# Performance work log

Hardware: AMD Instinct MI355X
Metric: run time of the kernel (lower is better)

## Reference

```python
import jax, jax.numpy as jnp
import numpy as np

MAX_POS = 8192
SOFT_CAP = 5.0


def rms_norm(x, scale, eps=1e-6):
    # RMSBatchNorm approximated as RMS normalization over channels with learned scale
    return x * jax.lax.rsqrt(jnp.mean(x * x, axis=-1, keepdims=True) + eps) * scale


def layer_norm(x, scale, offset, eps=1e-5):
    mean = jnp.mean(x, axis=-1, keepdims=True)
    var = jnp.mean(jnp.square(x - mean), axis=-1, keepdims=True)
    return (x - mean) * jax.lax.rsqrt(var + eps) * scale + offset


def apply_rope(x, max_position=MAX_POS):
    # x: [B, S, H, C]
    B, S, H, C = x.shape
    positions = jnp.arange(S, dtype=x.dtype).reshape(1, S)
    num_freq = C // 2
    inv_freq = (1.0 / (jnp.arange(num_freq) + jnp.geomspace(1, max_position - num_freq + 1, num_freq))).astype(x.dtype)
    theta = jnp.einsum('bs,f->bsf', positions, inv_freq)
    theta = jnp.repeat(theta, 2, axis=-1)[..., None, :]  # [1, S, 1, C]
    x_rotated = jnp.stack([-x[..., 1::2], x[..., ::2]], axis=-1).reshape(x.shape)
    return x * jnp.cos(theta) + x_rotated * jnp.sin(theta)


def setup_inputs() -> dict:
    key = jax.random.key(0)
    ks = jax.random.split(key, 16)
    B, S, D = 2, 2048, 1536
    H, CQK, CV = 8, 128, 192
    inp = {
        'x': jax.random.normal(ks[0], (B, S, D), jnp.float32),
        'attention_bias': jax.random.normal(ks[1], (B, H, S, S), jnp.float32),
        'rms_in_scale': jnp.ones((D,), jnp.float32),
        'wq': jax.random.normal(ks[2], (D, H * CQK), jnp.float32) / np.sqrt(D),
        'wk': jax.random.normal(ks[3], (D, CQK), jnp.float32) / np.sqrt(D),
        'wv': jax.random.normal(ks[4], (D, CV), jnp.float32) / np.sqrt(D),
        'q_scale': jnp.ones((CQK,), jnp.float32),
        'q_offset': jnp.zeros((CQK,), jnp.float32),
        'k_scale': jnp.ones((CQK,), jnp.float32),
        'k_offset': jnp.zeros((CQK,), jnp.float32),
        'v_scale': jnp.ones((CV,), jnp.float32),
        'v_offset': jnp.zeros((CV,), jnp.float32),
        'wo': jax.random.normal(ks[5], (H * CV, D), jnp.float32) / np.sqrt(H * CV),
        'bo': jnp.zeros((D,), jnp.float32),
        'rms_out_scale': jnp.ones((D,), jnp.float32),
    }
    return inp


def reference(x, attention_bias, rms_in_scale, wq, wk, wv, q_scale, q_offset,
              k_scale, k_offset, v_scale, v_offset, wo, bo, rms_out_scale):
    B, S, D = x.shape
    H, CQK, CV = 8, 128, 192
    h = rms_norm(x, rms_in_scale)
    q = layer_norm((h @ wq).reshape(B, S, H, CQK), q_scale, q_offset)
    k = layer_norm((h @ wk).reshape(B, S, 1, CQK), k_scale, k_offset)
    v = layer_norm((h @ wv).reshape(B, S, 1, CV), v_scale, v_offset)
    q = apply_rope(q)
    k = apply_rope(k)
    # MQA logits: single shared K head
    logits = jnp.einsum('bshc,bSc->bhsS', q, k[:, :, 0], preferred_element_type=jnp.float32)
    logits = logits / np.sqrt(128.0)
    logits = (logits + attention_bias).astype(jnp.float32)
    logits = jnp.tanh(logits / SOFT_CAP) * SOFT_CAP
    weights = jax.nn.softmax(logits, axis=-1)
    y = jnp.einsum('bhsS,bSc->bshc', weights, v[:, :, 0]).astype(q.dtype)
    y = y.reshape(B, S, H * CV) @ wo + bo
    return rms_norm(y, rms_out_scale)
```

## Files before the change

### kernel.cpp

```cpp
#include <hip/hip_runtime.h>
#include <hip/hip_bf16.h>

typedef unsigned short u16;
typedef short bf16x8 __attribute__((ext_vector_type(8)));
typedef float f32x4 __attribute__((ext_vector_type(4)));

#define NB 2
#define NS 2048
#define ND 1536
#define NH 8
#define NCQK 128
#define NCV 192
#define NBS 4096
#define NPAD 1408

__device__ __forceinline__ float bf2f(u16 u) {
  unsigned v = ((unsigned)u) << 16;
  return __builtin_bit_cast(float, v);
}
__device__ __forceinline__ u16 f2bf(float f) {
  unsigned u = __builtin_bit_cast(unsigned, f);
  u += 0x7fffu + ((u >> 16) & 1u);
  return (u16)(u >> 16);
}
__device__ __forceinline__ void glds16(const u16* g, u16* l) {
  __builtin_amdgcn_global_load_lds(
      (const __attribute__((address_space(1))) void*)g,
      (__attribute__((address_space(3))) void*)l, 16, 0, 0);
}
__device__ __forceinline__ f32x4 mfma16(bf16x8 a, bf16x8 b, f32x4 c) {
  return __builtin_amdgcn_mfma_f32_16x16x32_bf16(a, b, c, 0, 0, 0);
}

__global__ void transpose_k(const float* __restrict__ in, u16* __restrict__ out,
                            int K, int N) {
  __shared__ float t[64][65];
  const int n0 = blockIdx.x * 64, k0 = blockIdx.y * 64;
  const int tid = threadIdx.x;
  const int rl = tid >> 4, cl = (tid & 15) * 4;
  for (int p = 0; p < 4; p++) {
    int k = rl + p * 16;
    float4 v = *(const float4*)(in + (size_t)(k0 + k) * N + n0 + cl);
    t[k][cl] = v.x; t[k][cl + 1] = v.y; t[k][cl + 2] = v.z; t[k][cl + 3] = v.w;
  }
  __syncthreads();
  const int rn = tid >> 3, ck = (tid & 7) * 8;
  for (int p = 0; p < 2; p++) {
    int n = rn + p * 32;
    u16 tmp[8];
    for (int j = 0; j < 8; j++) tmp[j] = f2bf(t[ck + j][n]);
    *(uint4*)(out + (size_t)(n0 + n) * K + k0 + ck) = *(uint4*)tmp;
  }
}

__global__ void rmsnorm_in_k(const float* __restrict__ x, const float* __restrict__ scale,
                             u16* __restrict__ h) {
  __shared__ float sbuf[4];
  const int row = blockIdx.x, tid = threadIdx.x;
  const float* xr = x + (size_t)row * ND;
  float v[6]; float ss = 0.f;
  for (int i = 0; i < 6; i++) { v[i] = xr[tid + i * 256]; ss += v[i] * v[i]; }
  for (int o = 32; o; o >>= 1) ss += __shfl_xor(ss, o);
  if ((tid & 63) == 0) sbuf[tid >> 6] = ss;
  __syncthreads();
  ss = sbuf[0] + sbuf[1] + sbuf[2] + sbuf[3];
  const float inv = rsqrtf(ss * (1.f / ND) + 1e-6f);
  u16* hr = h + (size_t)row * ND;
  for (int i = 0; i < 6; i++) {
    int c = tid + i * 256;
    hr[c] = f2bf(v[i] * inv * scale[c]);
  }
}

template <bool F32OUT>
__global__ __launch_bounds__(256, 2)
void gemm_nt(const u16* __restrict__ A, const u16* __restrict__ Bt,
             float* __restrict__ Cf, u16* __restrict__ Cb, int M, int N, int K) {
  __shared__ __align__(16) u16 As[128 * 64];
  __shared__ __align__(16) u16 Bs[128 * 64];
  const int tid = threadIdx.x;
  const int wave = tid >> 6, lane = tid & 63, quad = lane >> 4, l16 = lane & 15;
  const int m0 = blockIdx.y * 128, n0 = blockIdx.x * 128;
  const int mrb = (wave & 1) * 4, nrb = (wave >> 1) * 4;
  f32x4 acc[4][4] = {};
  for (int k0 = 0; k0 < K; k0 += 64) {
    if (k0) __syncthreads();
    for (int i = 0; i < 4; i++) {
      int g = wave * 4 + i;
      int rb = g >> 1, kh = g & 1;
      int row = rb * 16 + l16, kc = kh * 4 + quad;
      glds16(A + (size_t)(m0 + row) * K + k0 + kc * 8, &As[(rb * 8 + kh * 4) * 128]);
      glds16(Bt + (size_t)(n0 + row) * K + k0 + kc * 8, &Bs[(rb * 8 + kh * 4) * 128]);
    }
    __syncthreads();
    for (int kk = 0; kk < 2; kk++) {
      bf16x8 af[4], bfr[4];
      for (int f = 0; f < 4; f++)
        af[f] = *(const bf16x8*)&As[(((mrb + f) * 8 + kk * 4 + quad) * 16 + l16) * 8];
      for (int f = 0; f < 4; f++)
        bfr[f] = *(const bf16x8*)&Bs[(((nrb + f) * 8 + kk * 4 + quad) * 16 + l16) * 8];
      for (int mf = 0; mf < 4; mf++)
        for (int nf = 0; nf < 4; nf++)
          acc[mf][nf] = mfma16(af[mf], bfr[nf], acc[mf][nf]);
    }
  }
  for (int mf = 0; mf < 4; mf++)
    for (int nf = 0; nf < 4; nf++)
      for (int r = 0; r < 4; r++) {
        int m = m0 + (wave & 1) * 64 + mf * 16 + quad * 4 + r;
        int n = n0 + (wave >> 1) * 64 + nf * 16 + l16;
        if (F32OUT) Cf[(size_t)m * N + n] = acc[mf][nf][r];
        else        Cb[(size_t)m * N + n] = f2bf(acc[mf][nf][r]);
      }
}

__global__ void ln_rope_k(const float* __restrict__ qkv,
                          const float* __restrict__ qs, const float* __restrict__ qo,
                          const float* __restrict__ ks, const float* __restrict__ ko,
                          const float* __restrict__ vs, const float* __restrict__ vo,
                          u16* __restrict__ Qg, u16* __restrict__ Kg, u16* __restrict__ Vg) {
  const int row = blockIdx.x;
  const int b = row >> 11, s = row & (NS - 1);
  const int wave = threadIdx.x >> 6, lane = threadIdx.x & 63;
  const float* base = qkv + (size_t)row * NPAD;
  const float gsp = __expf(logf(8129.f) * ((float)lane * (1.f / 63.f)));
  const float invf = 1.f / ((float)lane + gsp);
  float sn, cs;
  sincosf((float)s * invf, &sn, &cs);

  for (int hh = 0; hh < 2; hh++) {
    const int h = wave * 2 + hh;
    const float* p = base + h * NCQK;
    float x0 = p[lane * 2], x1 = p[lane * 2 + 1];
    float s1 = x0 + x1, s2 = x0 * x0 + x1 * x1;
    for (int o = 32; o; o >>= 1) { s1 += __shfl_xor(s1, o); s2 += __shfl_xor(s2, o); }
    float mean = s1 * (1.f / NCQK);
    float inv = rsqrtf(s2 * (1.f / NCQK) - mean * mean + 1e-5f);
    float y0 = (x0 - mean) * inv * qs[lane * 2] + qo[lane * 2];
    float y1 = (x1 - mean) * inv * qs[lane * 2 + 1] + qo[lane * 2 + 1];
    u16* dst = Qg + (size_t)row * (NH * NCQK) + h * NCQK + lane * 2;
    dst[0] = f2bf(y0 * cs - y1 * sn);
    dst[1] = f2bf(y1 * cs + y0 * sn);
  }
  if (wave == 0) {
    const float* p = base + NH * NCQK;
    float x0 = p[lane * 2], x1 = p[lane * 2 + 1];
    float s1 = x0 + x1, s2 = x0 * x0 + x1 * x1;
    for (int o = 32; o; o >>= 1) { s1 += __shfl_xor(s1, o); s2 += __shfl_xor(s2, o); }
    float mean = s1 * (1.f / NCQK);
    float inv = rsqrtf(s2 * (1.f / NCQK) - mean * mean + 1e-5f);
    float y0 = (x0 - mean) * inv * ks[lane * 2] + ko[lane * 2];
    float y1 = (x1 - mean) * inv * ks[lane * 2 + 1] + ko[lane * 2 + 1];
    u16* dst = Kg + (size_t)row * NCQK + lane * 2;
    dst[0] = f2bf(y0 * cs - y1 * sn);
    dst[1] = f2bf(y1 * cs + y0 * sn);
  }
  if (wave == 1) {
    const float* p = base + NH * NCQK + NCQK;
    float x[3]; float s1 = 0.f, s2 = 0.f;
    for (int i = 0; i < 3; i++) { x[i] = p[lane + i * 64]; s1 += x[i]; s2 += x[i] * x[i]; }
    for (int o = 32; o; o >>= 1) { s1 += __shfl_xor(s1, o); s2 += __shfl_xor(s2, o); }
    float mean = s1 * (1.f / NCV);
    float inv = rsqrtf(s2 * (1.f / NCV) - mean * mean + 1e-5f);
    for (int i = 0; i < 3; i++) {
      int c = lane + i * 64;
      float y = (x[i] - mean) * inv * vs[c] + vo[c];
      Vg[(size_t)(b * NCV + c) * NS + s] = f2bf(y);
    }
  }
}

__global__ __launch_bounds__(256, 3)
void attn_k(const u16* __restrict__ Qg, const u16* __restrict__ Kg,
            const u16* __restrict__ Vg, const float* __restrict__ bias,
            u16* __restrict__ Y) {
  __shared__ __align__(16) u16 Ks[64 * 128];
  __shared__ __align__(16) u16 Vs[192 * 64];
  __shared__ __align__(16) u16 Ps[64 * 64];
  const int tid = threadIdx.x;
  const int wave = tid >> 6, lane = tid & 63, quad = lane >> 4, l16 = lane & 15;
  const int s0 = blockIdx.x * 64;
  const int h = blockIdx.y, b = blockIdx.z;

  const float C1 = 0.0510069742f;
  const float C2 = 0.5770780163f;
  const float C3 = -14.4269504089f;
  const float C4 = 7.2134752044f;

  bf16x8 qa[4];
  {
    const u16* qr = Qg + ((size_t)((b * NS + s0 + wave * 16 + l16) * NH + h)) * NCQK;
#pragma unroll
    for (int kk = 0; kk < 4; kk++)
      qa[kk] = *(const bf16x8*)(qr + (kk * 4 + quad) * 8);
  }

  const u16* Kbase = Kg + (size_t)(b * NS) * NCQK;
  const u16* Vbase = Vg + (size_t)(b * NCV) * NS;
  const float* brow = bias + ((size_t)(b * NH + h) * NS + s0 + wave * 16) * NS;

#pragma unroll
  for (int i = 0; i < 4; i++)
    glds16(Kbase + (size_t)(wave * 16 + l16) * NCQK + (i * 4 + quad) * 8,
           &Ks[(wave * 16 + i * 4) * 128]);
#pragma unroll
  for (int i = 0; i < 6; i++) {
    int g = wave * 6 + i, cb = g >> 1, kh = g & 1;
    glds16(Vbase + (size_t)(cb * 16 + l16) * NS + (kh * 4 + quad) * 8,
           &Vs[(cb * 8 + kh * 4) * 128]);
  }
  float breg[16];
#pragma unroll
  for (int nb = 0; nb < 4; nb++)
#pragma unroll
    for (int r = 0; r < 4; r++)
      breg[nb * 4 + r] = brow[(size_t)(quad * 4 + r) * NS + nb * 16 + l16];
  __syncthreads();

  f32x4 oacc[12] = {};
  float lsum[4] = {0.f, 0.f, 0.f, 0.f};

  for (int kt = 0; kt < NS / 64; kt++) {
    f32x4 sacc[4] = {};
    __builtin_amdgcn_s_setprio(1);
#pragma unroll
    for (int kk = 0; kk < 4; kk++)
#pragma unroll
      for (int nb = 0; nb < 4; nb++) {
        bf16x8 kf = *(const bf16x8*)&Ks[((nb * 16 + kk * 4 + quad) * 16 + l16) * 8];
        sacc[nb] = mfma16(qa[kk], kf, sacc[nb]);
      }
    __builtin_amdgcn_s_setprio(0);

#pragma unroll
    for (int nb = 0; nb < 4; nb++) {
      const int key_l = nb * 16 + l16;
#pragma unroll
      for (int r = 0; r < 4; r++) {
        const int qrow = quad * 4 + r;
        float a = fmaf(sacc[nb][r], C1, breg[nb * 4 + r] * C2);
        float e2;
        asm("v_exp_f32 %0, %1" : "=v"(e2) : "v"(a));
        float u = __builtin_amdgcn_rcpf(e2 + 1.f);
        float a2 = fmaf(u, C3, C4);
        float p;
        asm("v_exp_f32 %0, %1" : "=v"(p) : "v"(a2));
        unsigned pk;
        asm("v_cvt_pk_bf16_f32 %0, %1, %2" : "=v"(pk) : "v"(p), "v"(p));
        lsum[r] += __builtin_bit_cast(float, pk << 16);
        Ps[((wave * 8 + (key_l >> 3)) * 16 + qrow) * 8 + (key_l & 7)] = (u16)pk;
      }
    }

    if (kt + 1 < NS / 64) {
      const int key0 = (kt + 1) * 64;
#pragma unroll
      for (int nb = 0; nb < 4; nb++)
#pragma unroll
        for (int r = 0; r < 4; r++)
          breg[nb * 4 + r] = brow[(size_t)(quad * 4 + r) * NS + key0 + nb * 16 + l16];
    }

    __builtin_amdgcn_s_setprio(1);
#pragma unroll
    for (int kk = 0; kk < 2; kk++) {
      bf16x8 pa = *(const bf16x8*)&Ps[((wave * 8 + kk * 4 + quad) * 16 + l16) * 8];
#pragma unroll
      for (int nb = 0; nb < 12; nb++) {
        bf16x8 vf = *(const bf16x8*)&Vs[((nb * 8 + kk * 4 + quad) * 16 + l16) * 8];
        oacc[nb] = mfma16(pa, vf, oacc[nb]);
      }
    }
    __builtin_amdgcn_s_setprio(0);

    if (kt + 1 < NS / 64) {
      const int key0 = (kt + 1) * 64;
      __syncthreads();
#pragma unroll
      for (int i = 0; i < 4; i++)
        glds16(Kbase + (size_t)(key0 + wave * 16 + l16) * NCQK + (i * 4 + quad) * 8,
               &Ks[(wave * 16 + i * 4) * 128]);
#pragma unroll
      for (int i = 0; i < 6; i++) {
        int g = wave * 6 + i, cb = g >> 1, kh = g & 1;
        glds16(Vbase + (size_t)(cb * 16 + l16) * NS + key0 + (kh * 4 + quad) * 8,
               &Vs[(cb * 8 + kh * 4) * 128]);
      }
      __syncthreads();
    }
  }

  for (int r = 0; r < 4; r++)
    for (int o = 1; o < 16; o <<= 1) lsum[r] += __shfl_xor(lsum[r], o);
  for (int r = 0; r < 4; r++) {
    const float inv = 1.f / lsum[r];
    const int m = s0 + wave * 16 + quad * 4 + r;
    u16* yr = Y + (size_t)(b * NS + m) * ND + h * NCV;
    for (int nb = 0; nb < 12; nb++) yr[nb * 16 + l16] = f2bf(oacc[nb][r] * inv);
  }
}

__global__ void final_k(const u16* __restrict__ yo, const float* __restrict__ bo,
                        const float* __restrict__ scale, float* __restrict__ out) {
  __shared__ float sbuf[4];
  const int row = blockIdx.x, tid = threadIdx.x;
  const u16* yr = yo + (size_t)row * ND;
  float v[6]; float ss = 0.f;
  for (int i = 0; i < 6; i++) {
    int c = tid + i * 256;
    v[i] = bf2f(yr[c]) + bo[c];
    ss += v[i] * v[i];
  }
  for (int o = 32; o; o >>= 1) ss += __shfl_xor(ss, o);
  if ((tid & 63) == 0) sbuf[tid >> 6] = ss;
  __syncthreads();
  ss = sbuf[0] + sbuf[1] + sbuf[2] + sbuf[3];
  const float inv = rsqrtf(ss * (1.f / ND) + 1e-6f);
  float* orow = out + (size_t)row * ND;
  for (int i = 0; i < 6; i++) {
    int c = tid + i * 256;
    orow[c] = v[i] * inv * scale[c];
  }
}

extern "C" void kernel_launch(void* const* d_in, const int* in_sizes, int n_in,
                              void* d_out, int out_size, void* d_ws, size_t ws_size,
                              hipStream_t stream) {
  const float* x    = (const float*)d_in[0];
  const float* bias = (const float*)d_in[1];
  const float* rin  = (const float*)d_in[2];
  const float* wq   = (const float*)d_in[3];
  const float* wk   = (const float*)d_in[4];
  const float* wv   = (const float*)d_in[5];
  const float* qsc  = (const float*)d_in[6];
  const float* qof  = (const float*)d_in[7];
  const float* ksc  = (const float*)d_in[8];
  const float* kof  = (const float*)d_in[9];
  const float* vsc  = (const float*)d_in[10];
  const float* vof  = (const float*)d_in[11];
  const float* wo   = (const float*)d_in[12];
  const float* bo   = (const float*)d_in[13];
  const float* rout = (const float*)d_in[14];

  char* ws = (char*)d_ws;
  size_t off = 0;
  auto alloc = [&](size_t bytes) -> void* {
    void* p = ws + off;
    off += (bytes + 255) & ~(size_t)255;
    return p;
  };
  u16*   h    = (u16*)alloc((size_t)NBS * ND * 2);
  u16*   wtq  = (u16*)alloc((size_t)NPAD * ND * 2);
  u16*   wto  = (u16*)alloc((size_t)ND * ND * 2);
  float* qkv  = (float*)alloc((size_t)NBS * NPAD * 4);
  u16*   Qb   = (u16*)alloc((size_t)NBS * NH * NCQK * 2);
  u16*   Kb   = (u16*)alloc((size_t)NBS * NCQK * 2);
  u16*   Vtb  = (u16*)alloc((size_t)NB * NCV * NS * 2);
  u16*   Ybf  = (u16*)alloc((size_t)NBS * ND * 2);
  u16*   Yob  = (u16*)alloc((size_t)NBS * ND * 2);

  transpose_k<<<dim3(16, 24), 256, 0, stream>>>(wq, wtq, ND, 1024);
  transpose_k<<<dim3(2, 24), 256, 0, stream>>>(wk, wtq + (size_t)1024 * ND, ND, 128);
  transpose_k<<<dim3(3, 24), 256, 0, stream>>>(wv, wtq + (size_t)1152 * ND, ND, 192);
  transpose_k<<<dim3(24, 24), 256, 0, stream>>>(wo, wto, ND, ND);
  rmsnorm_in_k<<<NBS, 256, 0, stream>>>(x, rin, h);
  gemm_nt<true><<<dim3(NPAD / 128, NBS / 128), 256, 0, stream>>>(h, wtq, qkv, nullptr, NBS, NPAD, ND);
  ln_rope_k<<<NBS, 256, 0, stream>>>(qkv, qsc, qof, ksc, kof, vsc, vof, Qb, Kb, Vtb);
  attn_k<<<dim3(NS / 64, NH, NB), 256, 0, stream>>>(Qb, Kb, Vtb, bias, Ybf);
  gemm_nt<false><<<dim3(ND / 128, NBS / 128), 256, 0, stream>>>(Ybf, wto, nullptr, Yob, NBS, ND, ND);
  final_k<<<NBS, 256, 0, stream>>>(Yob, bo, rout, (float*)d_out);
}
```

Measured before the change: 590.1 us.

## Split attention key tile across wave pairs with 2x2 register tiling and smem reduction

Reassigns attention work so each wave computes 32 query rows by 32 keys instead of 16 rows by 64 keys. Each loaded K and V fragment then feeds two MFMAs, which halves LDS fragment reads per MFMA. The two wave pairs each hold partial outputs over different key halves, and these are combined at the end through shared memory. This raises register use (launch bounds drop from 3 to 2 blocks per CU) and adds an extra reduction pass with syncs.

```diff
diff --git a/kernel.cpp b/kernel.cpp
--- a/kernel.cpp
+++ b/kernel.cpp
@@ -170,15 +170,18 @@
   }
 }
 
-__global__ __launch_bounds__(256, 3)
+__global__ __launch_bounds__(256, 2)
 void attn_k(const u16* __restrict__ Qg, const u16* __restrict__ Kg,
             const u16* __restrict__ Vg, const float* __restrict__ bias,
             u16* __restrict__ Y) {
-  __shared__ __align__(16) u16 Ks[64 * 128];
-  __shared__ __align__(16) u16 Vs[192 * 64];
-  __shared__ __align__(16) u16 Ps[64 * 64];
+  __shared__ __align__(16) u16 smem[24576];
+  __shared__ float lbuf[64];
+  u16* Ks = smem;
+  u16* Vs = smem + 8192;
+  u16* Ps = smem + 20480;
   const int tid = threadIdx.x;
   const int wave = tid >> 6, lane = tid & 63, quad = lane >> 4, l16 = lane & 15;
+  const int pair = wave >> 1, rw = wave & 1;
   const int s0 = blockIdx.x * 64;
   const int h = blockIdx.y, b = blockIdx.z;
 
@@ -187,17 +190,18 @@
   const float C3 = -14.4269504089f;
   const float C4 = 7.2134752044f;
 
-  bf16x8 qa[4];
-  {
-    const u16* qr = Qg + ((size_t)((b * NS + s0 + wave * 16 + l16) * NH + h)) * NCQK;
+  bf16x8 qa[2][4];
+#pragma unroll
+  for (int mf = 0; mf < 2; mf++) {
+    const u16* qr = Qg + ((size_t)((b * NS + s0 + rw * 32 + mf * 16 + l16) * NH + h)) * NCQK;
 #pragma unroll
     for (int kk = 0; kk < 4; kk++)
-      qa[kk] = *(const bf16x8*)(qr + (kk * 4 + quad) * 8);
+      qa[mf][kk] = *(const bf16x8*)(qr + (kk * 4 + quad) * 8);
   }
 
   const u16* Kbase = Kg + (size_t)(b * NS) * NCQK;
   const u16* Vbase = Vg + (size_t)(b * NCV) * NS;
-  const float* brow = bias + ((size_t)(b * NH + h) * NS + s0 + wave * 16) * NS;
+  const float* brow = bias + ((size_t)(b * NH + h) * NS + s0 + rw * 32) * NS + pair * 32 + l16;
 
 #pragma unroll
   for (int i = 0; i < 4; i++)
@@ -211,65 +215,72 @@
   }
   float breg[16];
 #pragma unroll
-  for (int nb = 0; nb < 4; nb++)
-#pragma unroll
-    for (int r = 0; r < 4; r++)
-      breg[nb * 4 + r] = brow[(size_t)(quad * 4 + r) * NS + nb * 16 + l16];
-  __syncthreads();
-
-  f32x4 oacc[12] = {};
-  float lsum[4] = {0.f, 0.f, 0.f, 0.f};
+  for (int mf = 0; mf < 2; mf++)
+#pragma unroll
+    for (int nb = 0; nb < 2; nb++)
+#pragma unroll
+      for (int r = 0; r < 4; r++)
+        breg[(mf * 2 + nb) * 4 + r] = brow[(size_t)(mf * 16 + quad * 4 + r) * NS + nb * 16];
+  __syncthreads();
+
+  f32x4 oacc[2][12] = {};
+  float lsum[8] = {};
+
+  const int pwb = wave * 1024;
 
   for (int kt = 0; kt < NS / 64; kt++) {
-    f32x4 sacc[4] = {};
+    f32x4 sacc[2][2] = {};
     __builtin_amdgcn_s_setprio(1);
 #pragma unroll
     for (int kk = 0; kk < 4; kk++)
 #pragma unroll
-      for (int nb = 0; nb < 4; nb++) {
-        bf16x8 kf = *(const bf16x8*)&Ks[((nb * 16 + kk * 4 + quad) * 16 + l16) * 8];
-        sacc[nb] = mfma16(qa[kk], kf, sacc[nb]);
+      for (int nb = 0; nb < 2; nb++) {
+        bf16x8 kf = *(const bf16x8*)&Ks[(((pair * 2 + nb) * 16 + kk * 4 + quad) * 16 + l16) * 8];
+        sacc[0][nb] = mfma16(qa[0][kk], kf, sacc[0][nb]);
+        sacc[1][nb] = mfma16(qa[1][kk], kf, sacc[1][nb]);
       }
     __builtin_amdgcn_s_setprio(0);
 
 #pragma unroll
-    for (int nb = 0; nb < 4; nb++) {
-      const int key_l = nb * 16 + l16;
-#pragma unroll
-      for (int r = 0; r < 4; r++) {
-        const int qrow = quad * 4 + r;
-        float a = fmaf(sacc[nb][r], C1, breg[nb * 4 + r] * C2);
-        float e2;
-        asm("v_exp_f32 %0, %1" : "=v"(e2) : "v"(a));
-        float u = __builtin_amdgcn_rcpf(e2 + 1.f);
-        float a2 = fmaf(u, C3, C4);
-        float p;
-        asm("v_exp_f32 %0, %1" : "=v"(p) : "v"(a2));
-        unsigned pk;
-        asm("v_cvt_pk_bf16_f32 %0, %1, %2" : "=v"(pk) : "v"(p), "v"(p));
-        lsum[r] += __builtin_bit_cast(float, pk << 16);
-        Ps[((wave * 8 + (key_l >> 3)) * 16 + qrow) * 8 + (key_l & 7)] = (u16)pk;
-      }
-    }
+    for (int mf = 0; mf < 2; mf++)
+#pragma unroll
+      for (int nb = 0; nb < 2; nb++) {
+        const int xk = nb * 16 + l16;
+#pragma unroll
+        for (int r = 0; r < 4; r++) {
+          float a = fmaf(sacc[mf][nb][r], C1, breg[(mf * 2 + nb) * 4 + r] * C2);
+          float e2;
+          asm("v_exp_f32 %0, %1" : "=v"(e2) : "v"(a));
+          float u = __builtin_amdgcn_rcpf(e2 + 1.f);
+          float a2 = fmaf(u, C3, C4);
+          float p;
+          asm("v_exp_f32 %0, %1" : "=v"(p) : "v"(a2));
+          unsigned pk;
+          asm("v_cvt_pk_bf16_f32 %0, %1, %2" : "=v"(pk) : "v"(p), "v"(p));
+          lsum[mf * 4 + r] += __builtin_bit_cast(float, pk << 16);
+          Ps[pwb + mf * 512 + (xk >> 3) * 128 + (quad * 4 + r) * 8 + (xk & 7)] = (u16)pk;
+        }
+      }
 
     if (kt + 1 < NS / 64) {
       const int key0 = (kt + 1) * 64;
 #pragma unroll
-      for (int nb = 0; nb < 4; nb++)
-#pragma unroll
-        for (int r = 0; r < 4; r++)
-          breg[nb * 4 + r] = brow[(size_t)(quad * 4 + r) * NS + key0 + nb * 16 + l16];
+      for (int mf = 0; mf < 2; mf++)
+#pragma unroll
+        for (int nb = 0; nb < 2; nb++)
+#pragma unroll
+          for (int r = 0; r < 4; r++)
+            breg[(mf * 2 + nb) * 4 + r] = brow[(size_t)(mf * 16 + quad * 4 + r) * NS + key0 + nb * 16];
     }
 
     __builtin_amdgcn_s_setprio(1);
-#pragma unroll
-    for (int kk = 0; kk < 2; kk++) {
-      bf16x8 pa = *(const bf16x8*)&Ps[((wave * 8 + kk * 4 + quad) * 16 + l16) * 8];
-#pragma unroll
-      for (int nb = 0; nb < 12; nb++) {
-        bf16x8 vf = *(const bf16x8*)&Vs[((nb * 8 + kk * 4 + quad) * 16 + l16) * 8];
-        oacc[nb] = mfma16(pa, vf, oacc[nb]);
-      }
+    bf16x8 pa0 = *(const bf16x8*)&Ps[pwb + quad * 128 + l16 * 8];
+    bf16x8 pa1 = *(const bf16x8*)&Ps[pwb + 512 + quad * 128 + l16 * 8];
+#pragma unroll
+    for (int nb = 0; nb < 12; nb++) {
+      bf16x8 vf = *(const bf16x8*)&Vs[((nb * 8 + pair * 4 + quad) * 16 + l16) * 8];
+      oacc[0][nb] = mfma16(pa0, vf, oacc[0][nb]);
+      oacc[1][nb] = mfma16(pa1, vf, oacc[1][nb]);
     }
     __builtin_amdgcn_s_setprio(0);
 
@@ -290,13 +301,38 @@
     }
   }
 
-  for (int r = 0; r < 4; r++)
-    for (int o = 1; o < 16; o <<= 1) lsum[r] += __shfl_xor(lsum[r], o);
-  for (int r = 0; r < 4; r++) {
-    const float inv = 1.f / lsum[r];
-    const int m = s0 + wave * 16 + quad * 4 + r;
-    u16* yr = Y + (size_t)(b * NS + m) * ND + h * NCV;
-    for (int nb = 0; nb < 12; nb++) yr[nb * 16 + l16] = f2bf(oacc[nb][r] * inv);
+#pragma unroll
+  for (int i = 0; i < 8; i++)
+    for (int o = 1; o < 16; o <<= 1) lsum[i] += __shfl_xor(lsum[i], o);
+
+  __syncthreads();
+  float* smemF = (float*)smem;
+  if (pair == 1) {
+#pragma unroll
+    for (int mf = 0; mf < 2; mf++) {
+#pragma unroll
+      for (int r = 0; r < 4; r++) {
+        const int row = rw * 32 + mf * 16 + quad * 4 + r;
+#pragma unroll
+        for (int nb = 0; nb < 12; nb++)
+          smemF[row * 192 + nb * 16 + l16] = oacc[mf][nb][r];
+        if (l16 == 0) lbuf[row] = lsum[mf * 4 + r];
+      }
+    }
+  }
+  __syncthreads();
+  if (pair == 0) {
+#pragma unroll
+    for (int mf = 0; mf < 2; mf++)
+#pragma unroll
+      for (int r = 0; r < 4; r++) {
+        const int row = rw * 32 + mf * 16 + quad * 4 + r;
+        const float inv = 1.f / (lsum[mf * 4 + r] + lbuf[row]);
+        u16* yr = Y + (size_t)(b * NS + s0 + row) * ND + h * NCV;
+#pragma unroll
+        for (int nb = 0; nb < 12; nb++)
+          yr[nb * 16 + l16] = f2bf((oacc[mf][nb][r] + smemF[row * 192 + nb * 16 + l16]) * inv);
+      }
   }
 }
 
```

Result: no change. 585.9 us (-0.7%).
